# Kernel optimization log

Measured on AMD Instinct MI355X. Metric: run time of the kernel, lower is better.

## Reference

```python
import jax, jax.numpy as jnp
import numpy as np
import math

S, B, L, D = 4096, 2048, 256, 128  # substructure pool, batch, max substructs/drug, hidden


def setup_inputs() -> dict:
    key = jax.random.key(0)
    ks = jax.random.split(key, 6)
    sub_feat = jax.random.normal(ks[0], (S, D), dtype=jnp.float32)
    sub_index = jax.random.randint(ks[1], (B, L), 0, S)
    # ragged lengths -> padded prefix mask (1.0 = valid substructure)
    lengths = jax.random.randint(ks[2], (B,), 8, L + 1)
    mask = (jnp.arange(L)[None, :] < lengths[:, None]).astype(jnp.float32)
    scale = 1.0 / math.sqrt(D)
    Wq = jax.random.normal(ks[3], (D, D), dtype=jnp.float32) * scale
    Wk = jax.random.normal(ks[4], (D, D), dtype=jnp.float32) * scale
    bq = jnp.zeros((D,), dtype=jnp.float32)
    bk = jnp.zeros((D,), dtype=jnp.float32)
    return {"sub_feat": sub_feat, "mask": mask, "Wq": Wq, "bq": bq,
            "Wk": Wk, "bk": bk, "sub_index": sub_index}


def reference(sub_feat, mask, Wq, bq, Wk, bk, sub_index):
    # per-drug gather of substructure ('expert') features: [B, L, D]
    gathered = sub_feat[sub_index]
    # single-head Q/K projections (V is computed but unused in the original)
    q = gathered @ Wq + bq  # [B, L, D]
    k = gathered @ Wk + bk  # [B, L, D]
    inv_sqrt_d = 1.0 / math.sqrt(D)
    # additive mask: (1 - m) * -10000 broadcast over query dim
    add_mask = (1.0 - mask)[:, None, :] * -10000.0  # [B, 1, L]
    scores = jnp.einsum('bid,bjd->bij', q, k) * inv_sqrt_d + add_mask  # [B, L, L]
    probs = jax.nn.softmax(scores, axis=-1)
    # O[:, 0, 0, :] in the original: head 0, query position 0
    score = probs[:, 0, :]  # [B, L]
    # drug_feat[i] = score[i] @ sub_feat[sub_index[i]]
    drug_embeddings = jnp.einsum('bl,bld->bd', score, gathered)  # [B, D]
    return drug_embeddings
```

## Files before the change

### kernel.cpp

```cpp
#include <hip/hip_runtime.h>
#include <hip/hip_cooperative_groups.h>

namespace cg = cooperative_groups;

#define DIM 128
#define LEN 256
#define INV_SQRT_D 0.08838834764831845f
#define LOG2E 1.4426950408889634f
#define SCALE_L2 (INV_SQRT_D * LOG2E)

#define WS_MT   0
#define WS_C    (DIM * DIM)
#define WS_W2   (DIM * DIM + DIM)
#define WS_BQBK (DIM * DIM + 2 * DIM)
#define WS_BF   (DIM * DIM + 2 * DIM + 8)

__device__ __forceinline__ float bl(unsigned u) { return __uint_as_float(u << 16); }
__device__ __forceinline__ float bh(unsigned u) { return __uint_as_float(u & 0xffff0000u); }

struct MainSmem {
    float2 ibw[LEN];
    float  g0L[DIM];
    float  vh[2][DIM];
    float  vL[DIM];
    float  OW[4][DIM];
    float  Zw[4];
    float  qbkL;
};

__device__ __forceinline__ void prep_unit(int unit, int t,
    const float* __restrict__ sub_feat,
    const float* __restrict__ Wq, const float* __restrict__ bq,
    const float* __restrict__ Wk, const float* __restrict__ bk,
    float* __restrict__ ws, ushort* __restrict__ bfb, int n4)
{
    if (unit < DIM) {
        __shared__ float wqj[DIM];
        if (t < DIM) wqj[t] = Wq[unit * DIM + t];
        __syncthreads();
        if (t < DIM) {
            const float4* row = reinterpret_cast<const float4*>(Wk + t * DIM);
            float acc = 0.f;
            #pragma unroll 8
            for (int i = 0; i < DIM / 4; ++i) {
                float4 u = row[i];
                acc = fmaf(u.x, wqj[4*i+0], acc);
                acc = fmaf(u.y, wqj[4*i+1], acc);
                acc = fmaf(u.z, wqj[4*i+2], acc);
                acc = fmaf(u.w, wqj[4*i+3], acc);
            }
            ws[WS_MT + unit * DIM + t] = acc;
        }
    } else if (unit == DIM) {
        __shared__ float bqs[DIM], bks[DIM], red[DIM];
        if (t < DIM) { bqs[t] = bq[t]; bks[t] = bk[t]; }
        __syncthreads();
        if (t < DIM) {
            const float4* rk = reinterpret_cast<const float4*>(Wk + t * DIM);
            const float4* rq = reinterpret_cast<const float4*>(Wq + t * DIM);
            float accC = 0.f, accW = 0.f;
            #pragma unroll 8
            for (int i = 0; i < DIM / 4; ++i) {
                float4 a  = rk[i];
                float4 b2 = rq[i];
                accC = fmaf(a.x,  bqs[4*i+0], accC);
                accC = fmaf(a.y,  bqs[4*i+1], accC);
                accC = fmaf(a.z,  bqs[4*i+2], accC);
                accC = fmaf(a.w,  bqs[4*i+3], accC);
                accW = fmaf(b2.x, bks[4*i+0], accW);
                accW = fmaf(b2.y, bks[4*i+1], accW);
                accW = fmaf(b2.z, bks[4*i+2], accW);
                accW = fmaf(b2.w, bks[4*i+3], accW);
            }
            ws[WS_C  + t] = accC;
            ws[WS_W2 + t] = accW;
            red[t] = bqs[t] * bks[t];
        }
        __syncthreads();
        if (t == 0) {
            float s = 0.f;
            for (int i = 0; i < DIM; ++i) s += red[i];
            ws[WS_BQBK] = s;
        }
    } else {
        const int i = (unit - DIM - 1) * 256 + t;
        if (i < n4) {
            const float4 u = reinterpret_cast<const float4*>(sub_feat)[i];
            ushort4 o;
            unsigned a;
            a = __float_as_uint(u.x); o.x = (ushort)((a + 0x7fffu + ((a >> 16) & 1u)) >> 16);
            a = __float_as_uint(u.y); o.y = (ushort)((a + 0x7fffu + ((a >> 16) & 1u)) >> 16);
            a = __float_as_uint(u.z); o.z = (ushort)((a + 0x7fffu + ((a >> 16) & 1u)) >> 16);
            a = __float_as_uint(u.w); o.w = (ushort)((a + 0x7fffu + ((a >> 16) & 1u)) >> 16);
            reinterpret_cast<ushort4*>(bfb)[i] = o;
        }
    }
}

__device__ __forceinline__ void stage_unit(int b, int t, MainSmem& sm,
    const float* __restrict__ sub_feat, const float* __restrict__ mask,
    const int* __restrict__ sub_index)
{
    const int   ij = sub_index[(size_t)b * LEN + t];
    const float mk = mask[(size_t)b * LEN + t];
    sm.ibw[t] = make_float2(__int_as_float(ij), (1.f - mk) * (-10000.f * LOG2E));
    if (t < 64) {
        const int r0 = sub_index[(size_t)b * LEN];
        const float2 g0p = reinterpret_cast<const float2*>(sub_feat + (size_t)r0 * DIM)[t];
        sm.g0L[2 * t]     = g0p.x;
        sm.g0L[2 * t + 1] = g0p.y;
    }
}

template<bool BF16>
__device__ __forceinline__ void main_rest(int b, int t, MainSmem& sm,
    const float* __restrict__ sub_feat, const ushort* __restrict__ gfeat,
    const float* __restrict__ ws, float* __restrict__ out)
{
    const int lane = t & 63;
    const int wv   = t >> 6;
    const int g    = lane >> 4;
    const int m16  = lane & 15;

    if (t < 64) {
        const float* w2 = ws + WS_W2;
        float qp = sm.g0L[2 * t] * w2[2 * t] + sm.g0L[2 * t + 1] * w2[2 * t + 1];
        #pragma unroll
        for (int o = 32; o > 0; o >>= 1) qp += __shfl_xor(qp, o);
        if (t == 0) sm.qbkL = (qp + ws[WS_BQBK]) * SCALE_L2;
    }
    {
        const int i  = t & (DIM - 1);
        const int hh = t >> 7;
        const float* Mrow = ws + WS_MT + hh * 64 * DIM;
        const float* gL   = sm.g0L + hh * 64;
        float a = 0.f;
        #pragma unroll 8
        for (int j = 0; j < 64; ++j)
            a = fmaf(gL[j], Mrow[j * DIM + i], a);
        sm.vh[hh][i] = a;
    }
    __syncthreads();
    if (t < DIM) sm.vL[t] = (sm.vh[0][t] + sm.vh[1][t] + ws[WS_C + t]) * SCALE_L2;
    __syncthreads();

    const float4 va = reinterpret_cast<const float4*>(sm.vL)[2 * m16];
    const float4 vb = reinterpret_cast<const float4*>(sm.vL)[2 * m16 + 1];
    const float qterm = sm.qbkL;

    float Zr = 0.f;
    float O0=0.f,O1=0.f,O2=0.f,O3=0.f,O4=0.f,O5=0.f,O6=0.f,O7=0.f;

    const int jbase = wv * 64;
    #pragma unroll 4
    for (int k = 0; k < 16; ++k) {
        const float2 ibp = sm.ibw[jbase + 4 * k + g];
        const int   ij = __float_as_int(ibp.x);
        const float bj = ibp.y;
        float f0, f1, f2, f3, f4, f5, f6, f7;
        if constexpr (BF16) {
            const uint4 u = *reinterpret_cast<const uint4*>(gfeat + (size_t)ij * DIM + 8 * m16);
            f0 = bl(u.x); f1 = bh(u.x); f2 = bl(u.y); f3 = bh(u.y);
            f4 = bl(u.z); f5 = bh(u.z); f6 = bl(u.w); f7 = bh(u.w);
        } else {
            const float* rp = sub_feat + (size_t)ij * DIM + 8 * m16;
            const float4 u0 = *reinterpret_cast<const float4*>(rp);
            const float4 u1 = *reinterpret_cast<const float4*>(rp + 4);
            f0 = u0.x; f1 = u0.y; f2 = u0.z; f3 = u0.w;
            f4 = u1.x; f5 = u1.y; f6 = u1.z; f7 = u1.w;
        }
        float sd = f0*va.x + f1*va.y + f2*va.z + f3*va.w
                 + f4*vb.x + f5*vb.y + f6*vb.z + f7*vb.w;
        sd += __shfl_xor(sd, 1);
        sd += __shfl_xor(sd, 2);
        sd += __shfl_xor(sd, 4);
        sd += __shfl_xor(sd, 8);
        const float e = exp2f(sd + qterm + bj);
        Zr += e;
        O0 = fmaf(e, f0, O0); O1 = fmaf(e, f1, O1);
        O2 = fmaf(e, f2, O2); O3 = fmaf(e, f3, O3);
        O4 = fmaf(e, f4, O4); O5 = fmaf(e, f5, O5);
        O6 = fmaf(e, f6, O6); O7 = fmaf(e, f7, O7);
    }

    #pragma unroll
    for (int msk = 16; msk <= 32; msk <<= 1) {
        Zr += __shfl_xor(Zr, msk);
        O0 += __shfl_xor(O0, msk); O1 += __shfl_xor(O1, msk);
        O2 += __shfl_xor(O2, msk); O3 += __shfl_xor(O3, msk);
        O4 += __shfl_xor(O4, msk); O5 += __shfl_xor(O5, msk);
        O6 += __shfl_xor(O6, msk); O7 += __shfl_xor(O7, msk);
    }
    if (lane < 16) {
        reinterpret_cast<float4*>(&sm.OW[wv][0])[2 * m16]     = make_float4(O0, O1, O2, O3);
        reinterpret_cast<float4*>(&sm.OW[wv][0])[2 * m16 + 1] = make_float4(O4, O5, O6, O7);
    }
    if (lane == 0) sm.Zw[wv] = Zr;
    __syncthreads();

    if (t < DIM) {
        const float Zt = sm.Zw[0] + sm.Zw[1] + sm.Zw[2] + sm.Zw[3];
        out[(size_t)b * DIM + t] =
            (sm.OW[0][t] + sm.OW[1][t] + sm.OW[2][t] + sm.OW[3][t]) / Zt;
    }
}

__global__ __launch_bounds__(256, 8) void coop_kernel(
    const float* __restrict__ sub_feat, const float* __restrict__ mask,
    const float* __restrict__ Wq, const float* __restrict__ bq,
    const float* __restrict__ Wk, const float* __restrict__ bk,
    const int* __restrict__ sub_index, float* __restrict__ ws,
    ushort* __restrict__ bfb, float* __restrict__ out, int n4)
{
    __shared__ MainSmem sm;
    const int t   = threadIdx.x;
    const int bid = blockIdx.x;
    const int nprep = DIM + 1 + (n4 + 255) / 256;

    if (bid < nprep) prep_unit(bid, t, sub_feat, Wq, bq, Wk, bk, ws, bfb, n4);
    stage_unit(bid, t, sm, sub_feat, mask, sub_index);
    if (bid < nprep) __threadfence();
    cg::this_grid().sync();

    main_rest<true>(bid, t, sm, sub_feat, bfb, ws, out);
}

__global__ __launch_bounds__(256) void prep_kernel(
    const float* __restrict__ sub_feat,
    const float* __restrict__ Wq, const float* __restrict__ bq,
    const float* __restrict__ Wk, const float* __restrict__ bk,
    float* __restrict__ ws, ushort* __restrict__ bfb, int n4)
{
    prep_unit(blockIdx.x, threadIdx.x, sub_feat, Wq, bq, Wk, bk, ws, bfb, n4);
}

__global__ __launch_bounds__(256, 8) void main_kernel_bf16(
    const float* __restrict__ sub_feat, const ushort* __restrict__ gfeat,
    const float* __restrict__ mask, const int* __restrict__ sub_index,
    const float* __restrict__ ws, float* __restrict__ out)
{
    __shared__ MainSmem sm;
    stage_unit(blockIdx.x, threadIdx.x, sm, sub_feat, mask, sub_index);
    __syncthreads();
    main_rest<true>(blockIdx.x, threadIdx.x, sm, sub_feat, gfeat, ws, out);
}

__global__ __launch_bounds__(256, 8) void main_kernel_f32(
    const float* __restrict__ sub_feat,
    const float* __restrict__ mask, const int* __restrict__ sub_index,
    const float* __restrict__ ws, float* __restrict__ out)
{
    __shared__ MainSmem sm;
    stage_unit(blockIdx.x, threadIdx.x, sm, sub_feat, mask, sub_index);
    __syncthreads();
    main_rest<false>(blockIdx.x, threadIdx.x, sm, sub_feat, nullptr, ws, out);
}

extern "C" void kernel_launch(void* const* d_in, const int* in_sizes, int n_in,
                              void* d_out, int out_size, void* d_ws, size_t ws_size,
                              hipStream_t stream) {
    const float* sub_feat  = (const float*)d_in[0];
    const float* mask      = (const float*)d_in[1];
    const float* Wq        = (const float*)d_in[2];
    const float* bq        = (const float*)d_in[3];
    const float* Wk        = (const float*)d_in[4];
    const float* bk        = (const float*)d_in[5];
    const int*   sub_index = (const int*)d_in[6];
    float* outp = (float*)d_out;
    float* ws   = (float*)d_ws;

    const int B  = in_sizes[6] / LEN;
    const int SD = in_sizes[0];
    int n4 = SD / 4;
    const int nprep = DIM + 1 + (n4 + 255) / 256;

    const size_t needed = ((size_t)WS_BF + (size_t)(SD + 1) / 2) * sizeof(float);
    const bool have_bf = (ws_size >= needed);

    bool coop = false;
    if (have_bf && B >= nprep) {
        int dev = 0;
        hipGetDevice(&dev);
        hipDeviceProp_t prop;
        if (hipGetDeviceProperties(&prop, dev) == hipSuccess && prop.cooperativeLaunch) {
            int maxb = 0;
            if (hipOccupancyMaxActiveBlocksPerMultiprocessor(
                    &maxb, reinterpret_cast<const void*>(coop_kernel), 256, 0) == hipSuccess &&
                (size_t)maxb * (size_t)prop.multiProcessorCount >= (size_t)B) {
                coop = true;
            }
        }
    }

    if (coop) {
        ushort* bfb = reinterpret_cast<ushort*>(ws + WS_BF);
        void* kargs[] = {
            (void*)&sub_feat, (void*)&mask, (void*)&Wq, (void*)&bq,
            (void*)&Wk, (void*)&bk, (void*)&sub_index, (void*)&ws,
            (void*)&bfb, (void*)&outp, (void*)&n4
        };
        hipLaunchCooperativeKernel(reinterpret_cast<const void*>(coop_kernel),
                                   dim3(B), dim3(256), kargs, 0, stream);
    } else if (have_bf) {
        ushort* bfb = reinterpret_cast<ushort*>(ws + WS_BF);
        prep_kernel<<<dim3(nprep), dim3(256), 0, stream>>>(
            sub_feat, Wq, bq, Wk, bk, ws, bfb, n4);
        main_kernel_bf16<<<dim3(B), dim3(256), 0, stream>>>(
            sub_feat, bfb, mask, sub_index, ws, outp);
    } else {
        prep_kernel<<<dim3(DIM + 1), dim3(256), 0, stream>>>(
            sub_feat, Wq, bq, Wk, bk, ws, nullptr, 0);
        main_kernel_f32<<<dim3(B), dim3(256), 0, stream>>>(
            sub_feat, mask, sub_index, ws, outp);
    }
}
```

Before: 29.38 us.

## Replace cooperative grid-sync kernel with batched per-drug query prep plus attention kernel

Removes the cooperative launch and grid-wide sync. The precomputed Wk^T·Wq matrix is replaced by a separate prep kernel that computes q0 and Wk·q0 per drug, batched 8 drugs per block, alongside the bf16 conversion of the feature table. The attention kernel then only loads a precomputed per-drug vector and scalar. The intent is to avoid grid-sync overhead and the per-block 128x64 matrix-vector over the shared M, at the cost of an extra kernel launch and writing B*D floats to workspace.

```diff
diff --git a/kernel.cpp b/kernel.cpp
--- a/kernel.cpp
+++ b/kernel.cpp
@@ -1,7 +1,4 @@
 #include <hip/hip_runtime.h>
-#include <hip/hip_cooperative_groups.h>
-
-namespace cg = cooperative_groups;
 
 #define DIM 128
 #define LEN 256
@@ -9,144 +6,26 @@
 #define LOG2E 1.4426950408889634f
 #define SCALE_L2 (INV_SQRT_D * LOG2E)
 
-#define WS_MT   0
-#define WS_C    (DIM * DIM)
-#define WS_W2   (DIM * DIM + DIM)
-#define WS_BQBK (DIM * DIM + 2 * DIM)
-#define WS_BF   (DIM * DIM + 2 * DIM + 8)
-
 __device__ __forceinline__ float bl(unsigned u) { return __uint_as_float(u << 16); }
 __device__ __forceinline__ float bh(unsigned u) { return __uint_as_float(u & 0xffff0000u); }
 
-struct MainSmem {
+struct AttnSmem {
     float2 ibw[LEN];
-    float  g0L[DIM];
-    float  vh[2][DIM];
-    float  vL[DIM];
     float  OW[4][DIM];
     float  Zw[4];
-    float  qbkL;
 };
 
-__device__ __forceinline__ void prep_unit(int unit, int t,
-    const float* __restrict__ sub_feat,
-    const float* __restrict__ Wq, const float* __restrict__ bq,
-    const float* __restrict__ Wk, const float* __restrict__ bk,
-    float* __restrict__ ws, ushort* __restrict__ bfb, int n4)
-{
-    if (unit < DIM) {
-        __shared__ float wqj[DIM];
-        if (t < DIM) wqj[t] = Wq[unit * DIM + t];
-        __syncthreads();
-        if (t < DIM) {
-            const float4* row = reinterpret_cast<const float4*>(Wk + t * DIM);
-            float acc = 0.f;
-            #pragma unroll 8
-            for (int i = 0; i < DIM / 4; ++i) {
-                float4 u = row[i];
-                acc = fmaf(u.x, wqj[4*i+0], acc);
-                acc = fmaf(u.y, wqj[4*i+1], acc);
-                acc = fmaf(u.z, wqj[4*i+2], acc);
-                acc = fmaf(u.w, wqj[4*i+3], acc);
-            }
-            ws[WS_MT + unit * DIM + t] = acc;
-        }
-    } else if (unit == DIM) {
-        __shared__ float bqs[DIM], bks[DIM], red[DIM];
-        if (t < DIM) { bqs[t] = bq[t]; bks[t] = bk[t]; }
-        __syncthreads();
-        if (t < DIM) {
-            const float4* rk = reinterpret_cast<const float4*>(Wk + t * DIM);
-            const float4* rq = reinterpret_cast<const float4*>(Wq + t * DIM);
-            float accC = 0.f, accW = 0.f;
-            #pragma unroll 8
-            for (int i = 0; i < DIM / 4; ++i) {
-                float4 a  = rk[i];
-                float4 b2 = rq[i];
-                accC = fmaf(a.x,  bqs[4*i+0], accC);
-                accC = fmaf(a.y,  bqs[4*i+1], accC);
-                accC = fmaf(a.z,  bqs[4*i+2], accC);
-                accC = fmaf(a.w,  bqs[4*i+3], accC);
-                accW = fmaf(b2.x, bks[4*i+0], accW);
-                accW = fmaf(b2.y, bks[4*i+1], accW);
-                accW = fmaf(b2.z, bks[4*i+2], accW);
-                accW = fmaf(b2.w, bks[4*i+3], accW);
-            }
-            ws[WS_C  + t] = accC;
-            ws[WS_W2 + t] = accW;
-            red[t] = bqs[t] * bks[t];
-        }
-        __syncthreads();
-        if (t == 0) {
-            float s = 0.f;
-            for (int i = 0; i < DIM; ++i) s += red[i];
-            ws[WS_BQBK] = s;
-        }
-    } else {
-        const int i = (unit - DIM - 1) * 256 + t;
-        if (i < n4) {
-            const float4 u = reinterpret_cast<const float4*>(sub_feat)[i];
-            ushort4 o;
-            unsigned a;
-            a = __float_as_uint(u.x); o.x = (ushort)((a + 0x7fffu + ((a >> 16) & 1u)) >> 16);
-            a = __float_as_uint(u.y); o.y = (ushort)((a + 0x7fffu + ((a >> 16) & 1u)) >> 16);
-            a = __float_as_uint(u.z); o.z = (ushort)((a + 0x7fffu + ((a >> 16) & 1u)) >> 16);
-            a = __float_as_uint(u.w); o.w = (ushort)((a + 0x7fffu + ((a >> 16) & 1u)) >> 16);
-            reinterpret_cast<ushort4*>(bfb)[i] = o;
-        }
-    }
-}
-
-__device__ __forceinline__ void stage_unit(int b, int t, MainSmem& sm,
-    const float* __restrict__ sub_feat, const float* __restrict__ mask,
-    const int* __restrict__ sub_index)
-{
-    const int   ij = sub_index[(size_t)b * LEN + t];
-    const float mk = mask[(size_t)b * LEN + t];
-    sm.ibw[t] = make_float2(__int_as_float(ij), (1.f - mk) * (-10000.f * LOG2E));
-    if (t < 64) {
-        const int r0 = sub_index[(size_t)b * LEN];
-        const float2 g0p = reinterpret_cast<const float2*>(sub_feat + (size_t)r0 * DIM)[t];
-        sm.g0L[2 * t]     = g0p.x;
-        sm.g0L[2 * t + 1] = g0p.y;
-    }
-}
-
 template<bool BF16>
-__device__ __forceinline__ void main_rest(int b, int t, MainSmem& sm,
+__device__ __forceinline__ void attn_core(
+    AttnSmem& sm, int t, int b,
+    const float4& va, const float4& vb, float qterm,
     const float* __restrict__ sub_feat, const ushort* __restrict__ gfeat,
-    const float* __restrict__ ws, float* __restrict__ out)
+    float* __restrict__ out)
 {
     const int lane = t & 63;
     const int wv   = t >> 6;
     const int g    = lane >> 4;
     const int m16  = lane & 15;
-
-    if (t < 64) {
-        const float* w2 = ws + WS_W2;
-        float qp = sm.g0L[2 * t] * w2[2 * t] + sm.g0L[2 * t + 1] * w2[2 * t + 1];
-        #pragma unroll
-        for (int o = 32; o > 0; o >>= 1) qp += __shfl_xor(qp, o);
-        if (t == 0) sm.qbkL = (qp + ws[WS_BQBK]) * SCALE_L2;
-    }
-    {
-        const int i  = t & (DIM - 1);
-        const int hh = t >> 7;
-        const float* Mrow = ws + WS_MT + hh * 64 * DIM;
-        const float* gL   = sm.g0L + hh * 64;
-        float a = 0.f;
-        #pragma unroll 8
-        for (int j = 0; j < 64; ++j)
-            a = fmaf(gL[j], Mrow[j * DIM + i], a);
-        sm.vh[hh][i] = a;
-    }
-    __syncthreads();
-    if (t < DIM) sm.vL[t] = (sm.vh[0][t] + sm.vh[1][t] + ws[WS_C + t]) * SCALE_L2;
-    __syncthreads();
-
-    const float4 va = reinterpret_cast<const float4*>(sm.vL)[2 * m16];
-    const float4 vb = reinterpret_cast<const float4*>(sm.vL)[2 * m16 + 1];
-    const float qterm = sm.qbkL;
 
     float Zr = 0.f;
     float O0=0.f,O1=0.f,O2=0.f,O3=0.f,O4=0.f,O5=0.f,O6=0.f,O7=0.f;
@@ -205,55 +84,214 @@
     }
 }
 
-__global__ __launch_bounds__(256, 8) void coop_kernel(
-    const float* __restrict__ sub_feat, const float* __restrict__ mask,
+__global__ __launch_bounds__(256) void prep2_kernel(
+    const float* __restrict__ sub_feat, const int* __restrict__ sub_index,
     const float* __restrict__ Wq, const float* __restrict__ bq,
     const float* __restrict__ Wk, const float* __restrict__ bk,
-    const int* __restrict__ sub_index, float* __restrict__ ws,
-    ushort* __restrict__ bfb, float* __restrict__ out, int n4)
-{
-    __shared__ MainSmem sm;
+    float* __restrict__ vout, float* __restrict__ qout,
+    ushort* __restrict__ bfb, int n4, int B, int nv)
+{
     const int t   = threadIdx.x;
     const int bid = blockIdx.x;
-    const int nprep = DIM + 1 + (n4 + 255) / 256;
-
-    if (bid < nprep) prep_unit(bid, t, sub_feat, Wq, bq, Wk, bk, ws, bfb, n4);
-    stage_unit(bid, t, sm, sub_feat, mask, sub_index);
-    if (bid < nprep) __threadfence();
-    cg::this_grid().sync();
-
-    main_rest<true>(bid, t, sm, sub_feat, bfb, ws, out);
-}
-
-__global__ __launch_bounds__(256) void prep_kernel(
-    const float* __restrict__ sub_feat,
+
+    if (bid >= nv) {
+        const int i = (bid - nv) * 256 + t;
+        if (i < n4) {
+            const float4 u = reinterpret_cast<const float4*>(sub_feat)[i];
+            ushort4 o;
+            unsigned a;
+            a = __float_as_uint(u.x); o.x = (ushort)((a + 0x7fffu + ((a >> 16) & 1u)) >> 16);
+            a = __float_as_uint(u.y); o.y = (ushort)((a + 0x7fffu + ((a >> 16) & 1u)) >> 16);
+            a = __float_as_uint(u.z); o.z = (ushort)((a + 0x7fffu + ((a >> 16) & 1u)) >> 16);
+            a = __float_as_uint(u.w); o.w = (ushort)((a + 0x7fffu + ((a >> 16) & 1u)) >> 16);
+            reinterpret_cast<ushort4*>(bfb)[i] = o;
+        }
+        return;
+    }
+
+    const int lane = t & 63;
+    const int wv   = t >> 6;
+    const int b0   = bid * 8;
+
+    __shared__ float g0[8][DIM];
+    __shared__ float ph[2][8][DIM];
+    __shared__ float q0[8][DIM];
+
+    #pragma unroll
+    for (int s = 0; s < 2; ++s) {
+        const int bb = wv * 2 + s;
+        const int b  = b0 + bb;
+        if (b < B) {
+            const int r0 = sub_index[(size_t)b * LEN];
+            const float2 p = reinterpret_cast<const float2*>(sub_feat + (size_t)r0 * DIM)[lane];
+            g0[bb][2 * lane]     = p.x;
+            g0[bb][2 * lane + 1] = p.y;
+        } else {
+            g0[bb][2 * lane] = 0.f; g0[bb][2 * lane + 1] = 0.f;
+        }
+    }
+    __syncthreads();
+
+    const int d = t & (DIM - 1);
+    const int h = t >> 7;
+
+    {
+        float acc[8] = {0.f,0.f,0.f,0.f,0.f,0.f,0.f,0.f};
+        const int e0 = h * 64;
+        #pragma unroll 4
+        for (int e = e0; e < e0 + 64; ++e) {
+            const float w = Wq[e * DIM + d];
+            #pragma unroll
+            for (int bb = 0; bb < 8; ++bb) acc[bb] = fmaf(g0[bb][e], w, acc[bb]);
+        }
+        #pragma unroll
+        for (int bb = 0; bb < 8; ++bb) ph[h][bb][d] = acc[bb];
+    }
+    __syncthreads();
+    if (h == 0) {
+        #pragma unroll
+        for (int bb = 0; bb < 8; ++bb) q0[bb][d] = ph[0][bb][d] + ph[1][bb][d] + bq[d];
+    }
+    __syncthreads();
+
+    #pragma unroll
+    for (int s = 0; s < 2; ++s) {
+        const int bb = wv * 2 + s;
+        float p = q0[bb][lane] * bk[lane] + q0[bb][lane + 64] * bk[lane + 64];
+        #pragma unroll
+        for (int o = 32; o > 0; o >>= 1) p += __shfl_xor(p, o);
+        if (lane == 0 && b0 + bb < B) qout[b0 + bb] = p * SCALE_L2;
+    }
+
+    {
+        float acc[8] = {0.f,0.f,0.f,0.f,0.f,0.f,0.f,0.f};
+        const int d0 = h * 64;
+        const float* wrow = Wk + (size_t)d * DIM + d0;
+        #pragma unroll 4
+        for (int dd = 0; dd < 64; ++dd) {
+            const float w = wrow[dd];
+            #pragma unroll
+            for (int bb = 0; bb < 8; ++bb) acc[bb] = fmaf(w, q0[bb][d0 + dd], acc[bb]);
+        }
+        #pragma unroll
+        for (int bb = 0; bb < 8; ++bb) ph[h][bb][d] = acc[bb];
+    }
+    __syncthreads();
+    if (h == 0) {
+        #pragma unroll
+        for (int bb = 0; bb < 8; ++bb) {
+            if (b0 + bb < B)
+                vout[(size_t)(b0 + bb) * DIM + d] = (ph[0][bb][d] + ph[1][bb][d]) * SCALE_L2;
+        }
+    }
+}
+
+__global__ __launch_bounds__(256, 8) void attn_bf16_kernel(
+    const ushort* __restrict__ gfeat, const float* __restrict__ mask,
+    const int* __restrict__ sub_index, const float* __restrict__ vbuf,
+    const float* __restrict__ qbuf, float* __restrict__ out)
+{
+    __shared__ AttnSmem sm;
+    const int t = threadIdx.x;
+    const int b = blockIdx.x;
+    const int m16 = (t & 63) & 15;
+
+    const int   ij = sub_index[(size_t)b * LEN + t];
+    const float mk = mask[(size_t)b * LEN + t];
+    sm.ibw[t] = make_float2(__int_as_float(ij), (1.f - mk) * (-10000.f * LOG2E));
+
+    const float4 va = reinterpret_cast<const float4*>(vbuf + (size_t)b * DIM)[2 * m16];
+    const float4 vb = reinterpret_cast<const float4*>(vbuf + (size_t)b * DIM)[2 * m16 + 1];
+    const float qterm = qbuf[b];
+
+    attn_core<true>(sm, t, b, va, vb, qterm, nullptr, gfeat, out);
+}
+
+__global__ __launch_bounds__(256, 8) void attn_f32_kernel(
+    const float* __restrict__ sub_feat, const float* __restrict__ mask,
+    const int* __restrict__ sub_index, const float* __restrict__ vbuf,
+    const float* __restrict__ qbuf, float* __restrict__ out)
+{
+    __shared__ AttnSmem sm;
+    const int t = threadIdx.x;
+    const int b = blockIdx.x;
+    const int m16 = (t & 63) & 15;
+
+    const int   ij = sub_index[(size_t)b * LEN + t];
+    const float mk = mask[(size_t)b * LEN + t];
+    sm.ibw[t] = make_float2(__int_as_float(ij), (1.f - mk) * (-10000.f * LOG2E));
+
+    const float4 va = reinterpret_cast<const float4*>(vbuf + (size_t)b * DIM)[2 * m16];
+    const float4 vb = reinterpret_cast<const float4*>(vbuf + (size_t)b * DIM)[2 * m16 + 1];
+    const float qterm = qbuf[b];
+
+    attn_core<false>(sm, t, b, va, vb, qterm, sub_feat, nullptr, out);
+}
+
+__global__ __launch_bounds__(256) void mono_kernel(
+    const float* __restrict__ sub_feat, const float* __restrict__ mask,
+    const int* __restrict__ sub_index,
     const float* __restrict__ Wq, const float* __restrict__ bq,
     const float* __restrict__ Wk, const float* __restrict__ bk,
-    float* __restrict__ ws, ushort* __restrict__ bfb, int n4)
-{
-    prep_unit(blockIdx.x, threadIdx.x, sub_feat, Wq, bq, Wk, bk, ws, bfb, n4);
-}
-
-__global__ __launch_bounds__(256, 8) void main_kernel_bf16(
-    const float* __restrict__ sub_feat, const ushort* __restrict__ gfeat,
-    const float* __restrict__ mask, const int* __restrict__ sub_index,
-    const float* __restrict__ ws, float* __restrict__ out)
-{
-    __shared__ MainSmem sm;
-    stage_unit(blockIdx.x, threadIdx.x, sm, sub_feat, mask, sub_index);
-    __syncthreads();
-    main_rest<true>(blockIdx.x, threadIdx.x, sm, sub_feat, gfeat, ws, out);
-}
-
-__global__ __launch_bounds__(256, 8) void main_kernel_f32(
-    const float* __restrict__ sub_feat,
-    const float* __restrict__ mask, const int* __restrict__ sub_index,
-    const float* __restrict__ ws, float* __restrict__ out)
-{
-    __shared__ MainSmem sm;
-    stage_unit(blockIdx.x, threadIdx.x, sm, sub_feat, mask, sub_index);
-    __syncthreads();
-    main_rest<false>(blockIdx.x, threadIdx.x, sm, sub_feat, nullptr, ws, out);
+    float* __restrict__ out)
+{
+    const int t    = threadIdx.x;
+    const int lane = t & 63;
+    const int b    = blockIdx.x;
+    const int m16  = lane & 15;
+
+    __shared__ AttnSmem sm;
+    __shared__ float g0L[DIM];
+    __shared__ float ph[2][DIM];
+    __shared__ float q0L[DIM];
+    __shared__ float vL[DIM];
+    __shared__ float qbkL;
+
+    {
+        const int   ij = sub_index[(size_t)b * LEN + t];
+        const float mk = mask[(size_t)b * LEN + t];
+        sm.ibw[t] = make_float2(__int_as_float(ij), (1.f - mk) * (-10000.f * LOG2E));
+    }
+    if (t < 64) {
+        const int r0 = sub_index[(size_t)b * LEN];
+        const float2 p = reinterpret_cast<const float2*>(sub_feat + (size_t)r0 * DIM)[t];
+        g0L[2 * t] = p.x; g0L[2 * t + 1] = p.y;
+    }
+    __syncthreads();
+
+    const int d = t & (DIM - 1);
+    const int h = t >> 7;
+    {
+        float a = 0.f;
+        const int e0 = h * 64;
+        #pragma unroll 4
+        for (int e = e0; e < e0 + 64; ++e) a = fmaf(g0L[e], Wq[e * DIM + d], a);
+        ph[h][d] = a;
+    }
+    __syncthreads();
+    if (h == 0) q0L[d] = ph[0][d] + ph[1][d] + bq[d];
+    __syncthreads();
+    if (t < 64) {
+        float p = q0L[t] * bk[t] + q0L[t + 64] * bk[t + 64];
+        #pragma unroll
+        for (int o = 32; o > 0; o >>= 1) p += __shfl_xor(p, o);
+        if (t == 0) qbkL = p * SCALE_L2;
+    }
+    {
+        float a = 0.f;
+        const int d0 = h * 64;
+        const float* wr = Wk + (size_t)d * DIM + d0;
+        #pragma unroll 4
+        for (int dd = 0; dd < 64; ++dd) a = fmaf(wr[dd], q0L[d0 + dd], a);
+        ph[h][d] = a;
+    }
+    __syncthreads();
+    if (h == 0) vL[d] = (ph[0][d] + ph[1][d]) * SCALE_L2;
+    __syncthreads();
+
+    const float4 va = reinterpret_cast<const float4*>(vL)[2 * m16];
+    const float4 vb = reinterpret_cast<const float4*>(vL)[2 * m16 + 1];
+    attn_core<false>(sm, t, b, va, vb, qbkL, sub_feat, nullptr, out);
 }
 
 extern "C" void kernel_launch(void* const* d_in, const int* in_sizes, int n_in,
@@ -271,46 +309,30 @@
 
     const int B  = in_sizes[6] / LEN;
     const int SD = in_sizes[0];
-    int n4 = SD / 4;
-    const int nprep = DIM + 1 + (n4 + 255) / 256;
-
-    const size_t needed = ((size_t)WS_BF + (size_t)(SD + 1) / 2) * sizeof(float);
-    const bool have_bf = (ws_size >= needed);
-
-    bool coop = false;
-    if (have_bf && B >= nprep) {
-        int dev = 0;
-        hipGetDevice(&dev);
-        hipDeviceProp_t prop;
-        if (hipGetDeviceProperties(&prop, dev) == hipSuccess && prop.cooperativeLaunch) {
-            int maxb = 0;
-            if (hipOccupancyMaxActiveBlocksPerMultiprocessor(
-                    &maxb, reinterpret_cast<const void*>(coop_kernel), 256, 0) == hipSuccess &&
-                (size_t)maxb * (size_t)prop.multiProcessorCount >= (size_t)B) {
-                coop = true;
-            }
-        }
-    }
-
-    if (coop) {
-        ushort* bfb = reinterpret_cast<ushort*>(ws + WS_BF);
-        void* kargs[] = {
-            (void*)&sub_feat, (void*)&mask, (void*)&Wq, (void*)&bq,
-            (void*)&Wk, (void*)&bk, (void*)&sub_index, (void*)&ws,
-            (void*)&bfb, (void*)&outp, (void*)&n4
-        };
-        hipLaunchCooperativeKernel(reinterpret_cast<const void*>(coop_kernel),
-                                   dim3(B), dim3(256), kargs, 0, stream);
-    } else if (have_bf) {
-        ushort* bfb = reinterpret_cast<ushort*>(ws + WS_BF);
-        prep_kernel<<<dim3(nprep), dim3(256), 0, stream>>>(
-            sub_feat, Wq, bq, Wk, bk, ws, bfb, n4);
-        main_kernel_bf16<<<dim3(B), dim3(256), 0, stream>>>(
-            sub_feat, bfb, mask, sub_index, ws, outp);
+    const int n4 = SD / 4;
+    const int nv = (B + 7) / 8;
+    const int ncv = (n4 + 255) / 256;
+
+    const size_t vq_floats  = (size_t)B * DIM + (size_t)B;
+    const size_t need_vq    = vq_floats * sizeof(float);
+    const size_t need_full  = need_vq + (size_t)SD * sizeof(ushort);
+
+    float*  vbuf = ws;
+    float*  qbuf = ws + (size_t)B * DIM;
+    ushort* bfb  = reinterpret_cast<ushort*>(ws + vq_floats);
+
+    if (ws_size >= need_full) {
+        prep2_kernel<<<dim3(nv + ncv), dim3(256), 0, stream>>>(
+            sub_feat, sub_index, Wq, bq, Wk, bk, vbuf, qbuf, bfb, n4, B, nv);
+        attn_bf16_kernel<<<dim3(B), dim3(256), 0, stream>>>(
+            bfb, mask, sub_index, vbuf, qbuf, outp);
+    } else if (ws_size >= need_vq) {
+        prep2_kernel<<<dim3(nv), dim3(256), 0, stream>>>(
+            sub_feat, sub_index, Wq, bq, Wk, bk, vbuf, qbuf, nullptr, 0, B, nv);
+        attn_f32_kernel<<<dim3(B), dim3(256), 0, stream>>>(
+            sub_feat, mask, sub_index, vbuf, qbuf, outp);
     } else {
-        prep_kernel<<<dim3(DIM + 1), dim3(256), 0, stream>>>(
-            sub_feat, Wq, bq, Wk, bk, ws, nullptr, 0);
-        main_kernel_f32<<<dim3(B), dim3(256), 0, stream>>>(
-            sub_feat, mask, sub_index, ws, outp);
-    }
-}
+        mono_kernel<<<dim3(B), dim3(256), 0, stream>>>(
+            sub_feat, mask, sub_index, Wq, bq, Wk, bk, outp);
+    }
+}
```

After: 27.85 us. -5.2%, faster.
